# Kernel optimization log

Hardware: AMD Instinct MI355X
Metric: run time of the kernel (lower is better)

Reference implementation:

```python
import jax, jax.numpy as jnp
import numpy as np

TEMP = 0.07  # temperature used as logits / 0.07 in the original


def setup_inputs() -> dict:
    key = jax.random.key(0)
    k1, k2, k3 = jax.random.split(key, 3)
    B, N, T, L, D = 8, 128, 8, 6, 256
    meta = jax.random.normal(k1, (B, N, T, L, D), dtype=jnp.float32)
    thing = jax.random.randint(k2, (B, N, T), 0, 2, dtype=jnp.int32)
    label = jax.random.randint(k3, (B, N, T), 0, 40, dtype=jnp.int32)
    return {"meta_weight_for_con": meta, "thing_gt_idx": thing, "label_tmp": label}


def _con_loss(meta, thing, label):
    # meta: [B,N,T,L,D]; thing,label: [B,N,T]
    B, N, T, L, D = meta.shape
    P = N * T
    valid = thing.reshape(B, P).astype(bool)            # [B,P] boolean gt mask
    lab = label.reshape(B, P)                           # [B,P]
    # meta_weight_b[mask] -> [K,L,D]; permute(1,0,2) -> per-layer [K,D].
    # We keep all P positions and mask instead of compacting (jit-friendly).
    w = meta.reshape(B, P, L, D).transpose(0, 2, 1, 3)  # [B,L,P,D]
    w = w / jnp.maximum(jnp.linalg.norm(w, axis=-1, keepdims=True), 1e-12)  # F.normalize
    z = jnp.einsum('blpd,blqd->blpq', w, w) / TEMP      # similarity / temp [B,L,P,P]

    same = lab[:, :, None] == lab[:, None, :]           # [B,P,P]
    vpair = valid[:, :, None] & valid[:, None, :]
    eye = jnp.eye(P, dtype=bool)
    pos_mask = same & (~eye) & vpair                    # positives: same label, not self
    neg_mask = (~same) & vpair                          # negatives: different label

    K = valid.sum(axis=1)                               # [B] ins_num_ per batch
    pos_count = pos_mask.sum(axis=-1)                   # [B,P]
    neg_count = neg_mask.sum(axis=-1)                   # [B,P]

    # --- random positive sample per (batch, layer, row), mirroring np.random.choice ---
    u = jax.random.uniform(jax.random.key(42), (B, L, P))
    r = jnp.floor(u * pos_count[:, None, :].astype(u.dtype)).astype(jnp.int32)
    r = jnp.minimum(r, jnp.maximum(pos_count - 1, 0)[:, None, :])
    ranks = jnp.cumsum(pos_mask, axis=-1) - 1           # rank of each positive in index order
    sel = pos_mask[:, None, :, :] & (ranks[:, None, :, :] == r[..., None])  # [B,L,P,P]
    zp = jnp.sum(jnp.where(sel, z, 0.0), axis=-1)       # chosen positive logit [B,L,P]
    diag = jnp.diagonal(z, axis1=-2, axis2=-1)          # self-sim fallback when no positives
    zp = jnp.where((pos_count > 0)[:, None, :], zp, diag)

    # --- last negative (original pads by repeating the last negative to K-1) ---
    iota = jnp.arange(P)
    idx_last = jnp.max(jnp.where(neg_mask, iota[None, None, :], -1), axis=-1)  # [B,P]
    idx = jnp.broadcast_to(jnp.maximum(idx_last, 0)[:, None, :, None], (B, L, P, 1))
    zl = jnp.take_along_axis(z, idx, axis=-1)[..., 0]   # [B,L,P]

    # --- stable CE with label 0: loss = lse(logits) - zp ---
    max_n = jnp.max(jnp.where(neg_mask[:, None], z, -jnp.inf), axis=-1)  # [B,L,P]
    m = jnp.maximum(zp, max_n)
    m = jnp.where(jnp.isfinite(m), m, zp)
    sum_neg = jnp.sum(jnp.where(neg_mask[:, None], jnp.exp(z - m[..., None]), 0.0), axis=-1)
    pad = jnp.maximum((K[:, None] - 1 - neg_count), 0).astype(z.dtype)   # [B,P]
    pad_term = pad[:, None, :] * jnp.where((neg_count > 0)[:, None, :], jnp.exp(zl - m), 0.0)
    loss_row = m + jnp.log(jnp.exp(zp - m) + sum_neg + pad_term) - zp    # [B,L,P]

    row_w = valid.astype(z.dtype)
    mean_per = jnp.sum(loss_row * row_w[:, None, :], axis=-1) / jnp.maximum(K, 1)[:, None].astype(z.dtype)  # [B,L]

    gate = jnp.sum((thing.sum(axis=2) > 0), axis=1) >= 2  # skip batches with <2 gt rows
    return jnp.sum(jnp.where(gate[:, None], mean_per, 0.0))


def reference(meta_weight_for_con, thing_gt_idx, label_tmp):
    return _con_loss(meta_weight_for_con, thing_gt_idx, label_tmp)
```

## Files before the change

### kernel.cpp

```cpp
#include <hip/hip_runtime.h>
#include <stdint.h>

namespace {

constexpr int Bb = 8, Ll = 6, Dd = 256, Pp = 1024;
constexpr float SCALE_Y = 14.285714285714286f * 1.4426950408889634f;
constexpr float M0y = 21.0f;
constexpr float LN2f = 0.6931471805599453f;

typedef __attribute__((ext_vector_type(8))) short short8;
typedef __attribute__((ext_vector_type(4))) float floatx4;

__device__ __forceinline__ void async16(const void* g, void* l) {
  __builtin_amdgcn_global_load_lds(
      (const __attribute__((address_space(1))) void*)g,
      (__attribute__((address_space(3))) void*)l, 16, 0, 0);
}

__device__ __forceinline__ uint32_t rotl32(uint32_t x, int n) {
  return (x << n) | (x >> (32 - n));
}
__device__ __forceinline__ void tf_round(uint32_t& x0, uint32_t& x1, int r) {
  x0 += x1; x1 = rotl32(x1, r); x1 ^= x0;
}
__device__ void threefry2x32(uint32_t x0, uint32_t x1, uint32_t& o0, uint32_t& o1) {
  const uint32_t k0 = 0u, k1 = 42u;
  const uint32_t k2 = k0 ^ k1 ^ 0x1BD11BDAu;
  x0 += k0; x1 += k1;
  tf_round(x0,x1,13); tf_round(x0,x1,15); tf_round(x0,x1,26); tf_round(x0,x1,6);
  x0 += k1; x1 += k2 + 1u;
  tf_round(x0,x1,17); tf_round(x0,x1,29); tf_round(x0,x1,16); tf_round(x0,x1,24);
  x0 += k2; x1 += k0 + 2u;
  tf_round(x0,x1,13); tf_round(x0,x1,15); tf_round(x0,x1,26); tf_round(x0,x1,6);
  x0 += k0; x1 += k1 + 3u;
  tf_round(x0,x1,17); tf_round(x0,x1,29); tf_round(x0,x1,16); tf_round(x0,x1,24);
  x0 += k1; x1 += k2 + 4u;
  tf_round(x0,x1,13); tf_round(x0,x1,15); tf_round(x0,x1,26); tf_round(x0,x1,6);
  x0 += k2; x1 += k0 + 5u;
  o0 = x0; o1 = x1;
}
__device__ float jax_u01(uint32_t idx) {
  const uint32_t HALF = (uint32_t)(Bb * Ll * Pp / 2);
  uint32_t o0, o1, bits;
  if (idx < HALF) { threefry2x32(idx, idx + HALF, o0, o1); bits = o0; }
  else            { threefry2x32(idx - HALF, idx, o0, o1); bits = o1; }
  return __uint_as_float((bits >> 9) | 0x3f800000u) - 1.0f;
}

__device__ __forceinline__ unsigned short bf16rne(float x) {
  uint32_t u = __float_as_uint(x);
  return (unsigned short)((u + 0x7FFFu + ((u >> 16) & 1u)) >> 16);
}

constexpr int NB_NORM = Bb * Pp * Ll / 4;
constexpr int NB_ROW  = Bb * Pp / 4;

__global__ void prep_k(const float* __restrict__ meta, const int* __restrict__ thing,
                       const int* __restrict__ label, unsigned short* __restrict__ wn,
                       int* __restrict__ qpos, int* __restrict__ negc,
                       int* __restrict__ qidx, int* __restrict__ Kv,
                       int* __restrict__ gatev, float* __restrict__ rowsum_g,
                       float* __restrict__ out) {
  __shared__ int sK[256], sG[256];
  const int bid = blockIdx.x, t = threadIdx.x;

  if (bid < NB_NORM) {
    const int wid = (bid * 256 + t) >> 6;
    const int lane = t & 63;
    const float4 v = *(const float4*)(meta + (size_t)wid * Dd + lane * 4);
    float ss = v.x * v.x + v.y * v.y + v.z * v.z + v.w * v.w;
    #pragma unroll
    for (int m = 32; m; m >>= 1) ss += __shfl_xor(ss, m, 64);
    const float inv = 1.0f / fmaxf(sqrtf(ss), 1e-12f);
    const int bp = wid / Ll, l = wid - bp * Ll;
    const int b = bp >> 10, p = bp & (Pp - 1);
    unsigned short* dst = wn + ((size_t)(b * Ll + l) * Pp + p) * Dd + lane * 4;
    ushort4 o;
    o.x = bf16rne(v.x * inv); o.y = bf16rne(v.y * inv);
    o.z = bf16rne(v.z * inv); o.w = bf16rne(v.w * inv);
    *(ushort4*)dst = o;
    return;
  }
  if (bid < NB_NORM + NB_ROW) {
    const int wid = (bid - NB_NORM) * 4 + (t >> 6);
    const int lane = t & 63;
    const int b = wid >> 10, p = wid & (Pp - 1);
    const int* lab = label + b * Pp;
    const int* th  = thing + b * Pp;
    const int myLab = lab[p];
    const bool myValid = (th[p] != 0);

    uint32_t posbits = 0;
    int cnt[16];
    int pc = 0, nc = 0, last = -1;
    #pragma unroll
    for (int c = 0; c < 16; ++c) {
      const int q = c * 64 + lane;
      const int lq = lab[q];
      const bool vq = (th[q] != 0);
      const bool same = (lq == myLab);
      const bool pos = myValid && vq && same && (q != p);
      const bool neg = myValid && vq && !same;
      uint64_t bp2 = __ballot(pos);
      uint64_t bn = __ballot(neg);
      if (pos) posbits |= (1u << c);
      cnt[c] = __popcll(bp2);
      pc += cnt[c];
      nc += __popcll(bn);
      if (bn) last = c * 64 + 63 - __clzll(bn);
    }
    int qsel[Ll];
    #pragma unroll
    for (int l = 0; l < Ll; ++l) qsel[l] = p;
    if (pc > 0) {
      for (int l = 0; l < Ll; ++l) {
        const float u = jax_u01((uint32_t)((b * Ll + l) * Pp + p));
        int r = (int)floorf(u * (float)pc);
        r = min(r, pc - 1);
        int base = 0;
        for (int c = 0; c < 16; ++c) {
          if (r < base + cnt[c]) {
            const bool mine = (posbits >> c) & 1u;
            uint64_t bm = __ballot(mine);
            uint64_t ltmask = (lane == 0) ? 0ull : (~0ull >> (64 - lane));
            int myrank = __popcll(bm & ltmask);
            bool hit = mine && (base + myrank == r);
            uint64_t hb = __ballot(hit);
            qsel[l] = c * 64 + (int)__builtin_ctzll(hb);
            break;
          }
          base += cnt[c];
        }
      }
    }
    if (lane == 0) {
      negc[wid] = nc;
      qidx[wid] = (last < 0) ? 0 : last;
      #pragma unroll
      for (int l = 0; l < Ll; ++l) qpos[(b * Ll + l) * Pp + p] = qsel[l];
    }
    return;
  }
  if (bid < NB_NORM + NB_ROW + Bb) {
    const int b = bid - (NB_NORM + NB_ROW);
    int k = 0;
    for (int p = t; p < Pp; p += 256) k += (thing[b * Pp + p] != 0);
    int g = 0;
    if (t < 128) {
      int any = 0;
      for (int tt = 0; tt < 8; ++tt) any |= (thing[(b * 128 + t) * 8 + tt] != 0);
      g = any;
    }
    sK[t] = k; sG[t] = g;
    __syncthreads();
    for (int s = 128; s; s >>= 1) {
      if (t < s) { sK[t] += sK[t + s]; sG[t] += sG[t + s]; }
      __syncthreads();
    }
    if (t == 0) { Kv[b] = sK[0]; gatev[b] = (sG[0] >= 2) ? 1 : 0; }
    return;
  }
  if (bid < NB_NORM + NB_ROW + Bb + 48) {
    const int idx = (bid - (NB_NORM + NB_ROW + Bb)) * 256 + t;
    *(float4*)(rowsum_g + idx * 4) = (float4){0.f, 0.f, 0.f, 0.f};
    return;
  }
  if (t == 0) out[0] = 0.f;
}

__global__ __launch_bounds__(256)
void gemm_loss_k(const unsigned short* __restrict__ wn,
                 const int* __restrict__ thing, const int* __restrict__ label,
                 const int* __restrict__ qpos, const int* __restrict__ qidx,
                 float* __restrict__ rowsum_g, float* __restrict__ zp_g,
                 float* __restrict__ zl_g) {
  __shared__ __align__(16) unsigned short As[128 * 64];
  __shared__ __align__(16) unsigned short Bs[128 * 64];
  __shared__ int labp_s[128], qpos_s[128], qidx_s[128], clab_s[128], cval_s[128];
  __shared__ float rowsum_lds[128];

  const int t = threadIdx.x;
  const int bl = blockIdx.z;
  const int b = bl / Ll;
  const int p0 = blockIdx.x * 128, q0 = blockIdx.y * 128;

  if (t < 128) {
    labp_s[t] = label[b * Pp + p0 + t];
    qpos_s[t] = qpos[bl * Pp + p0 + t];
    qidx_s[t] = qidx[b * Pp + p0 + t];
    clab_s[t] = label[b * Pp + q0 + t];
    cval_s[t] = thing[b * Pp + q0 + t];
    rowsum_lds[t] = 0.f;
  }

  const unsigned short* Wbl = wn + (size_t)bl * Pp * Dd;
  const int lane = t & 63;
  const int w = t >> 6, wr = w >> 1, wc = w & 1;
  const int cq = lane & 15, rq = lane >> 4;
  const int wbase16 = (t & ~63) * 16;

  floatx4 acc[4][4];
  #pragma unroll
  for (int i = 0; i < 4; ++i)
    #pragma unroll
    for (int j = 0; j < 4; ++j) acc[i][j] = (floatx4){0.f, 0.f, 0.f, 0.f};

  for (int k0 = 0; k0 < Dd; k0 += 64) {
    __syncthreads();
    #pragma unroll
    for (int it = 0; it < 4; ++it) {
      const int c = it * 256 + t;
      const int row = c >> 3, sp = c & 7;
      const int sl = sp ^ (row & 7);
      const char* lbase = (const char*)0 + it * 4096 + wbase16;
      async16(Wbl + (size_t)(p0 + row) * Dd + k0 + sl * 8, (char*)As + it * 4096 + wbase16);
      async16(Wbl + (size_t)(q0 + row) * Dd + k0 + sl * 8, (char*)Bs + it * 4096 + wbase16);
      (void)lbase;
    }
    __syncthreads();
    #pragma unroll
    for (int sub = 0; sub < 2; ++sub) {
      short8 af[4], bf[4];
      #pragma unroll
      for (int fi = 0; fi < 4; ++fi) {
        const int row = wr * 64 + fi * 16 + cq;
        const int sp = (sub * 4 + rq) ^ (row & 7);
        af[fi] = *(const short8*)((const char*)As + row * 128 + sp * 16);
      }
      #pragma unroll
      for (int fj = 0; fj < 4; ++fj) {
        const int row = wc * 64 + fj * 16 + cq;
        const int sp = (sub * 4 + rq) ^ (row & 7);
        bf[fj] = *(const short8*)((const char*)Bs + row * 128 + sp * 16);
      }
      #pragma unroll
      for (int fi = 0; fi < 4; ++fi)
        #pragma unroll
        for (int fj = 0; fj < 4; ++fj)
          acc[fi][fj] = __builtin_amdgcn_mfma_f32_16x16x32_bf16(af[fi], bf[fj],
                                                                acc[fi][fj], 0, 0, 0);
    }
  }

  int qcol[4], qlabv[4];
  float qvalf[4];
  #pragma unroll
  for (int fj = 0; fj < 4; ++fj) {
    const int cl = wc * 64 + fj * 16 + cq;
    qcol[fj] = q0 + cl;
    qlabv[fj] = clab_s[cl];
    qvalf[fj] = cval_s[cl] ? 1.f : 0.f;
  }
  #pragma unroll
  for (int fi = 0; fi < 4; ++fi) {
    #pragma unroll
    for (int reg = 0; reg < 4; ++reg) {
      const int rl = wr * 64 + fi * 16 + rq * 4 + reg;
      const int rlab = labp_s[rl];
      const int rqp = qpos_s[rl], rqi = qidx_s[rl];
      float rsum = 0.f;
      #pragma unroll
      for (int fj = 0; fj < 4; ++fj) {
        const float y = acc[fi][fj][reg] * SCALE_Y;
        const float negm = (qlabv[fj] != rlab) ? qvalf[fj] : 0.f;
        rsum += negm * exp2f(y - M0y);
        if (qcol[fj] == rqp) zp_g[bl * Pp + p0 + rl] = y;
        if (qcol[fj] == rqi) zl_g[bl * Pp + p0 + rl] = y;
      }
      rsum += __shfl_xor(rsum, 1); rsum += __shfl_xor(rsum, 2);
      rsum += __shfl_xor(rsum, 4); rsum += __shfl_xor(rsum, 8);
      if (cq == 0) atomicAdd(&rowsum_lds[rl], rsum);
    }
  }
  __syncthreads();
  if (t < 128) atomicAdd(&rowsum_g[bl * Pp + p0 + t], rowsum_lds[t]);
}

__global__ void finalize_k(const float* __restrict__ rowsum_g, const float* __restrict__ zp_g,
                           const float* __restrict__ zl_g, const int* __restrict__ negc,
                           const int* __restrict__ thing, const int* __restrict__ Kv,
                           const int* __restrict__ gatev, float* __restrict__ out) {
  const int bl = blockIdx.x, b = bl / Ll, t = threadIdx.x;
  const int Kb = Kv[b];
  const float invK = 1.f / (float)max(Kb, 1);
  float acc = 0.f;
  for (int p = t; p < Pp; p += 256) {
    if (thing[b * Pp + p] != 0) {
      const float yp = zp_g[bl * Pp + p], yl = zl_g[bl * Pp + p];
      const float rs = rowsum_g[bl * Pp + p];
      const int nc = negc[b * Pp + p];
      const float pad = fmaxf((float)(Kb - 1 - nc), 0.f);
      const float tot = exp2f(yp - M0y) + rs + ((nc > 0) ? pad * exp2f(yl - M0y) : 0.f);
      acc += LN2f * (M0y + log2f(tot) - yp) * invK;
    }
  }
  __shared__ float sb[256];
  sb[t] = acc;
  __syncthreads();
  for (int s = 128; s; s >>= 1) {
    if (t < s) sb[t] += sb[t + s];
    __syncthreads();
  }
  if (t == 0 && gatev[b]) atomicAdd(out, sb[0]);
}

}

extern "C" void kernel_launch(void* const* d_in, const int* in_sizes, int n_in,
                              void* d_out, int out_size, void* d_ws, size_t ws_size,
                              hipStream_t stream) {
  const float* meta = (const float*)d_in[0];
  const int* thing  = (const int*)d_in[1];
  const int* label  = (const int*)d_in[2];
  float* out = (float*)d_out;

  char* ws = (char*)d_ws;
  size_t off = 0;
  unsigned short* wn = (unsigned short*)(ws + off); off += (size_t)Bb * Ll * Pp * Dd * 2;
  int* qpos  = (int*)(ws + off); off += (size_t)Bb * Ll * Pp * 4;
  int* negc  = (int*)(ws + off); off += (size_t)Bb * Pp * 4;
  int* qidx  = (int*)(ws + off); off += (size_t)Bb * Pp * 4;
  int* Kv    = (int*)(ws + off); off += 64;
  int* gatev = (int*)(ws + off); off += 64;
  float* rowsum_g = (float*)(ws + off); off += (size_t)Bb * Ll * Pp * 4;
  float* zp_g     = (float*)(ws + off); off += (size_t)Bb * Ll * Pp * 4;
  float* zl_g     = (float*)(ws + off); off += (size_t)Bb * Ll * Pp * 4;

  const int nb_prep = NB_NORM + NB_ROW + Bb + 48 + 1;
  prep_k<<<nb_prep, 256, 0, stream>>>(meta, thing, label, wn, qpos, negc, qidx,
                                      Kv, gatev, rowsum_g, out);
  {
    dim3 grid(Pp / 128, Pp / 128, Bb * Ll);
    gemm_loss_k<<<grid, 256, 0, stream>>>(wn, thing, label, qpos, qidx,
                                          rowsum_g, zp_g, zl_g);
  }
  finalize_k<<<Bb * Ll, 256, 0, stream>>>(rowsum_g, zp_g, zl_g, negc, thing, Kv, gatev, out);
}
```

Baseline: 168.0 us.

## Exploit Gram matrix symmetry by computing only upper-triangular tiles

The similarity matrix is symmetric, so the GEMM grid now covers only the 36 upper-triangular 128x128 tile pairs per (batch, layer) instead of all 64. Each off-diagonal tile contributes both row sums and column sums, and writes the positive and last-index logits for both the row and column positions. Diagonal tiles load a single operand tile and reuse it for both MFMA inputs. The row validity mask is now folded into the negative term so the transposed contribution stays correct. This roughly halves the MFMA and load work, at the cost of extra column reductions, more atomics and an occupancy hint in the launch bounds.

```diff
diff --git a/kernel.cpp b/kernel.cpp
--- a/kernel.cpp
+++ b/kernel.cpp
@@ -10,6 +10,17 @@
 
 typedef __attribute__((ext_vector_type(8))) short short8;
 typedef __attribute__((ext_vector_type(4))) float floatx4;
+
+__device__ const int PAIRS[36] = {
+  0x00,0x01,0x02,0x03,0x04,0x05,0x06,0x07,
+  0x11,0x12,0x13,0x14,0x15,0x16,0x17,
+  0x22,0x23,0x24,0x25,0x26,0x27,
+  0x33,0x34,0x35,0x36,0x37,
+  0x44,0x45,0x46,0x47,
+  0x55,0x56,0x57,
+  0x66,0x67,
+  0x77
+};
 
 __device__ __forceinline__ void async16(const void* g, void* l) {
   __builtin_amdgcn_global_load_lds(
@@ -168,7 +179,7 @@
   if (t == 0) out[0] = 0.f;
 }
 
-__global__ __launch_bounds__(256)
+__global__ __launch_bounds__(256, 4)
 void gemm_loss_k(const unsigned short* __restrict__ wn,
                  const int* __restrict__ thing, const int* __restrict__ label,
                  const int* __restrict__ qpos, const int* __restrict__ qidx,
@@ -176,21 +187,29 @@
                  float* __restrict__ zl_g) {
   __shared__ __align__(16) unsigned short As[128 * 64];
   __shared__ __align__(16) unsigned short Bs[128 * 64];
-  __shared__ int labp_s[128], qpos_s[128], qidx_s[128], clab_s[128], cval_s[128];
-  __shared__ float rowsum_lds[128];
+  __shared__ int labp_s[128], valp_s[128], qposP_s[128], qidxP_s[128];
+  __shared__ int labq_s[128], valq_s[128], qposQ_s[128], qidxQ_s[128];
+  __shared__ float rowsum_lds[128], colsum_lds[128];
 
   const int t = threadIdx.x;
-  const int bl = blockIdx.z;
+  const int bl = blockIdx.y;
   const int b = bl / Ll;
-  const int p0 = blockIdx.x * 128, q0 = blockIdx.y * 128;
+  const int pair = PAIRS[blockIdx.x];
+  const int pt = pair >> 4, qt = pair & 15;
+  const bool diag = (pt == qt);
+  const int p0 = pt * 128, q0 = qt * 128;
 
   if (t < 128) {
-    labp_s[t] = label[b * Pp + p0 + t];
-    qpos_s[t] = qpos[bl * Pp + p0 + t];
-    qidx_s[t] = qidx[b * Pp + p0 + t];
-    clab_s[t] = label[b * Pp + q0 + t];
-    cval_s[t] = thing[b * Pp + q0 + t];
+    labp_s[t]  = label[b * Pp + p0 + t];
+    valp_s[t]  = thing[b * Pp + p0 + t];
+    qposP_s[t] = qpos[bl * Pp + p0 + t];
+    qidxP_s[t] = qidx[b * Pp + p0 + t];
+    labq_s[t]  = label[b * Pp + q0 + t];
+    valq_s[t]  = thing[b * Pp + q0 + t];
+    qposQ_s[t] = qpos[bl * Pp + q0 + t];
+    qidxQ_s[t] = qidx[b * Pp + q0 + t];
     rowsum_lds[t] = 0.f;
+    colsum_lds[t] = 0.f;
   }
 
   const unsigned short* Wbl = wn + (size_t)bl * Pp * Dd;
@@ -205,6 +224,8 @@
     #pragma unroll
     for (int j = 0; j < 4; ++j) acc[i][j] = (floatx4){0.f, 0.f, 0.f, 0.f};
 
+  const char* Bbase = diag ? (const char*)As : (const char*)Bs;
+
   for (int k0 = 0; k0 < Dd; k0 += 64) {
     __syncthreads();
     #pragma unroll
@@ -212,10 +233,9 @@
       const int c = it * 256 + t;
       const int row = c >> 3, sp = c & 7;
       const int sl = sp ^ (row & 7);
-      const char* lbase = (const char*)0 + it * 4096 + wbase16;
       async16(Wbl + (size_t)(p0 + row) * Dd + k0 + sl * 8, (char*)As + it * 4096 + wbase16);
-      async16(Wbl + (size_t)(q0 + row) * Dd + k0 + sl * 8, (char*)Bs + it * 4096 + wbase16);
-      (void)lbase;
+      if (!diag)
+        async16(Wbl + (size_t)(q0 + row) * Dd + k0 + sl * 8, (char*)Bs + it * 4096 + wbase16);
     }
     __syncthreads();
     #pragma unroll
@@ -231,7 +251,7 @@
       for (int fj = 0; fj < 4; ++fj) {
         const int row = wc * 64 + fj * 16 + cq;
         const int sp = (sub * 4 + rq) ^ (row & 7);
-        bf[fj] = *(const short8*)((const char*)Bs + row * 128 + sp * 16);
+        bf[fj] = *(const short8*)(Bbase + row * 128 + sp * 16);
       }
       #pragma unroll
       for (int fi = 0; fi < 4; ++fi)
@@ -242,14 +262,17 @@
     }
   }
 
-  int qcol[4], qlabv[4];
+  int qcol[4], qlabv[4], cqp[4], cqi[4];
   float qvalf[4];
+  float csum[4] = {0.f, 0.f, 0.f, 0.f};
   #pragma unroll
   for (int fj = 0; fj < 4; ++fj) {
     const int cl = wc * 64 + fj * 16 + cq;
     qcol[fj] = q0 + cl;
-    qlabv[fj] = clab_s[cl];
-    qvalf[fj] = cval_s[cl] ? 1.f : 0.f;
+    qlabv[fj] = labq_s[cl];
+    qvalf[fj] = valq_s[cl] ? 1.f : 0.f;
+    cqp[fj] = qposQ_s[cl];
+    cqi[fj] = qidxQ_s[cl];
   }
   #pragma unroll
   for (int fi = 0; fi < 4; ++fi) {
@@ -257,23 +280,42 @@
     for (int reg = 0; reg < 4; ++reg) {
       const int rl = wr * 64 + fi * 16 + rq * 4 + reg;
       const int rlab = labp_s[rl];
-      const int rqp = qpos_s[rl], rqi = qidx_s[rl];
+      const float rvalf = valp_s[rl] ? 1.f : 0.f;
+      const int rqp = qposP_s[rl], rqi = qidxP_s[rl];
+      const int prow = p0 + rl;
       float rsum = 0.f;
       #pragma unroll
       for (int fj = 0; fj < 4; ++fj) {
         const float y = acc[fi][fj][reg] * SCALE_Y;
-        const float negm = (qlabv[fj] != rlab) ? qvalf[fj] : 0.f;
-        rsum += negm * exp2f(y - M0y);
-        if (qcol[fj] == rqp) zp_g[bl * Pp + p0 + rl] = y;
-        if (qcol[fj] == rqi) zl_g[bl * Pp + p0 + rl] = y;
+        const float negm = (qlabv[fj] != rlab) ? (qvalf[fj] * rvalf) : 0.f;
+        const float term = negm * exp2f(y - M0y);
+        rsum += term;
+        csum[fj] += term;
+        if (qcol[fj] == rqp) zp_g[bl * Pp + prow] = y;
+        if (qcol[fj] == rqi) zl_g[bl * Pp + prow] = y;
+        if (!diag) {
+          if (prow == cqp[fj]) zp_g[bl * Pp + qcol[fj]] = y;
+          if (prow == cqi[fj]) zl_g[bl * Pp + qcol[fj]] = y;
+        }
       }
       rsum += __shfl_xor(rsum, 1); rsum += __shfl_xor(rsum, 2);
       rsum += __shfl_xor(rsum, 4); rsum += __shfl_xor(rsum, 8);
       if (cq == 0) atomicAdd(&rowsum_lds[rl], rsum);
     }
   }
+  if (!diag) {
+    #pragma unroll
+    for (int fj = 0; fj < 4; ++fj) {
+      float c = csum[fj];
+      c += __shfl_xor(c, 16); c += __shfl_xor(c, 32);
+      if (rq == 0) atomicAdd(&colsum_lds[wc * 64 + fj * 16 + cq], c);
+    }
+  }
   __syncthreads();
-  if (t < 128) atomicAdd(&rowsum_g[bl * Pp + p0 + t], rowsum_lds[t]);
+  if (t < 128) {
+    atomicAdd(&rowsum_g[bl * Pp + p0 + t], rowsum_lds[t]);
+    if (!diag) atomicAdd(&rowsum_g[bl * Pp + q0 + t], colsum_lds[t]);
+  }
 }
 
 __global__ void finalize_k(const float* __restrict__ rowsum_g, const float* __restrict__ zp_g,
@@ -330,7 +372,7 @@
   prep_k<<<nb_prep, 256, 0, stream>>>(meta, thing, label, wn, qpos, negc, qidx,
                                       Kv, gatev, rowsum_g, out);
   {
-    dim3 grid(Pp / 128, Pp / 128, Bb * Ll);
+    dim3 grid(36, Bb * Ll);
     gemm_loss_k<<<grid, 256, 0, stream>>>(wn, thing, label, qpos, qidx,
                                           rowsum_g, zp_g, zl_g);
   }
```

After: 184.5 us. +9.8%, slower.
